# Optimization experiments

Hardware: AMD Instinct MI355X
Metric: run time of the kernel (lower is better)

## Reference

```python
import jax, jax.numpy as jnp
import numpy as np

B, T, C, H = 256, 256, 512, 64  # batch, seq, n_embd, head_size


def setup_inputs() -> dict:
    key = jax.random.key(0)
    kx, kk, kq, kv = jax.random.split(key, 4)
    x = jax.random.normal(kx, (B, T, C), dtype=jnp.float32)
    # nn.Linear(C, H, bias=False): store as [C, H] so y = x @ W
    Wk = jax.random.normal(kk, (C, H), dtype=jnp.float32) * (C ** -0.5)
    Wq = jax.random.normal(kq, (C, H), dtype=jnp.float32) * (C ** -0.5)
    Wv = jax.random.normal(kv, (C, H), dtype=jnp.float32) * (C ** -0.5)
    return {"x": x, "Wk": Wk, "Wq": Wq, "Wv": Wv}


def reference(x, Wk, Wq, Wv):
    Bx, Tx, Cx = x.shape
    k = jnp.einsum('btc,ch->bth', x, Wk)
    q = jnp.einsum('btc,ch->bth', x, Wq)
    v = jnp.einsum('btc,ch->bth', x, Wv)
    # NOTE: original scales by C**-0.5 (embed dim), not head_size**-0.5
    wei = jnp.einsum('bth,bsh->bts', q, k) * (Cx ** -0.5)  # [B,T,T]
    causal = jnp.tril(jnp.ones((Tx, Tx), dtype=bool))
    wei = jnp.where(causal, wei, -jnp.inf)
    wei = jax.nn.softmax(wei, axis=-1)
    # dropout is identity at inference (deterministic reference)
    out = jnp.einsum('bts,bsh->bth', wei, v)  # [B,T,H]
    return out
```

## Files before the change

kernel.cpp:

```cpp
#include <hip/hip_runtime.h>

#define BB 256
#define TT 256
#define CC 512
#define HH 64

typedef __bf16 bf16;
typedef __bf16 bf16x4 __attribute__((ext_vector_type(4)));
typedef __bf16 bf16x8 __attribute__((ext_vector_type(8)));
typedef float  f32x4  __attribute__((ext_vector_type(4)));

#define MFMA16(a, b, c) __builtin_amdgcn_mfma_f32_16x16x32_bf16((a), (b), (c), 0, 0, 0)

typedef __attribute__((address_space(1))) const void cas1_void;
typedef __attribute__((address_space(3))) void as3_void;
__device__ __forceinline__ void g2lds16(const void* g, void* l) {
    __builtin_amdgcn_global_load_lds((cas1_void*)g, (as3_void*)l, 16, 0, 0);
}

__global__ __launch_bounds__(256) void wtrans(const float* __restrict__ Wk,
                                              const float* __restrict__ Wq,
                                              const float* __restrict__ Wv,
                                              bf16* __restrict__ wt) {
    int which = blockIdx.y;
    const float* W = (which == 0) ? Wq : (which == 1) ? Wk : Wv;
    int idx = blockIdx.x * 256 + threadIdx.x;
    int n = idx & 63, k4 = idx >> 6;
    bf16x4 o;
    #pragma unroll
    for (int i = 0; i < 4; ++i) o[i] = (bf16)W[(k4 * 4 + i) * HH + n];
    *(bf16x4*)(&wt[which * (CC * HH) + n * CC + k4 * 4]) = o;
}

__global__ __launch_bounds__(1024) void fused(const float* __restrict__ x,
                                              const bf16* __restrict__ wt,
                                              float* __restrict__ out) {
    __shared__ __align__(16) char smem[135168];
    const int tid  = threadIdx.x;
    const int wv   = tid >> 6;
    const int lane = tid & 63;
    const int quad = lane >> 4;
    const int l15  = lane & 15;
    const int l7   = l15 & 7;
    const int l3   = l15 & 3;
    const int b    = blockIdx.x;
    const float* xg = x + (size_t)b * TT * CC;

    auto stage = [&](int p, int kc) {
        char* xbase = smem + p * 32768;
        #pragma unroll
        for (int j = 0; j < 2; ++j) {
            int s = j * 1024 + tid;
            int r = s >> 3, up = s & 7;
            int u = up ^ (r & 7);
            const float* gp = xg + (size_t)r * CC + kc * 32 + u * 4;
            g2lds16(gp, xbase + (j * 1024 + wv * 64) * 16);
        }
        if (wv < 12) {
            char* wbase = smem + 98304 + p * 12288;
            int n = wv * 16 + (lane >> 2);
            int u = (lane & 3) ^ (n & 3);
            const bf16* gp = wt + (size_t)n * CC + kc * 32 + u * 8;
            g2lds16(gp, wbase + wv * 1024);
        }
    };

    f32x4 acc[12];
    #pragma unroll
    for (int nt = 0; nt < 12; ++nt) acc[nt] = (f32x4){0.f, 0.f, 0.f, 0.f};

    stage(0, 0);
    int pc = 0;
    for (int kc = 0; kc < 16; ++kc) {
        int pn = (pc == 2) ? 0 : pc + 1;
        if (kc < 15) {
            stage(pn, kc + 1);
            if (wv < 12) asm volatile("s_waitcnt vmcnt(3)" ::: "memory");
            else         asm volatile("s_waitcnt vmcnt(2)" ::: "memory");
        } else {
            asm volatile("s_waitcnt vmcnt(0)" ::: "memory");
        }
        __builtin_amdgcn_s_barrier();

        const char* xbase = smem + pc * 32768;
        const char* wbase = smem + 98304 + pc * 12288;
        int row = wv * 16 + l15;
        const char* rp = xbase + row * 128;
        f32x4 x0 = *(const f32x4*)(rp + (((quad * 2)     ^ l7) * 16));
        f32x4 x1 = *(const f32x4*)(rp + (((quad * 2 + 1) ^ l7) * 16));
        bf16x8 a0;
        #pragma unroll
        for (int j = 0; j < 4; ++j) {
            a0[j] = (bf16)x0[j]; a0[j + 4] = (bf16)x1[j];
        }
        #pragma unroll
        for (int nt = 0; nt < 12; ++nt) {
            int n = (nt >> 2) * 64 + (nt & 3) * 16 + l15;
            const char* np = wbase + n * 64;
            bf16x8 b0 = *(const bf16x8*)(np + ((quad ^ l3) * 16));
            acc[nt] = MFMA16(a0, b0, acc[nt]);
        }
        pc = pn;
    }
    __syncthreads();

    bf16* qs = (bf16*)smem;
    bf16* ks = (bf16*)(smem + 32768);
    bf16* vs = (bf16*)(smem + 65536);
    const float scale = 0.044194173824159216f;
    {
        int gt = wv * 16 + quad * 4;
        #pragma unroll
        for (int nt = 0; nt < 12; ++nt) {
            int h = (nt & 3) * 16 + l15;
            int wch = nt >> 2;
            if (wch == 0) {
                #pragma unroll
                for (int r = 0; r < 4; ++r) {
                    int row = gt + r;
                    *(bf16*)((char*)qs + row * 128 + (((h >> 3) ^ (row & 7)) * 16)
                             + (h & 7) * 2) = (bf16)(acc[nt][r] * scale);
                }
            } else if (wch == 1) {
                #pragma unroll
                for (int r = 0; r < 4; ++r) {
                    int row = gt + r;
                    *(bf16*)((char*)ks + row * 128 + (((h >> 3) ^ (row & 7)) * 16)
                             + (h & 7) * 2) = (bf16)(acc[nt][r]);
                }
            } else {
                bf16x4 pv;
                #pragma unroll
                for (int r = 0; r < 4; ++r) pv[r] = (bf16)(acc[nt][r]);
                *(bf16x4*)((char*)vs + h * 512 + (((gt >> 3) ^ (h & 31)) * 16)
                           + ((gt >> 2) & 1) * 8) = pv;
            }
        }
    }
    __syncthreads();

    bf16* pb = (bf16*)(smem + 98304 + wv * 2048);
    const int w0 = wv & 1, w1 = (wv >> 1) & 1, w2 = (wv >> 2) & 1, w3 = wv >> 3;
    const int rt = (w3 << 3) | ((w1 ^ w3) << 2) | (w2 << 1) | (w0 ^ w2);
    const int rowbase = rt * 16;
    const int ctmax = rt;
    const int t = rowbase + l15;

    const char* qp = (const char*)qs + t * 128;
    bf16x8 bq0 = *(const bf16x8*)(qp + ((quad ^ l7) * 16));
    bf16x8 bq1 = *(const bf16x8*)(qp + (((4 + quad) ^ l7) * 16));

    float m_run = -3.0e38f, sm = 0.f;
    f32x4 o[4];
    #pragma unroll
    for (int ht = 0; ht < 4; ++ht) o[ht] = (f32x4){0.f, 0.f, 0.f, 0.f};

    #pragma unroll
    for (int qp4 = 0; qp4 < 4; ++qp4) {
        if (qp4 * 4 <= ctmax) {
            f32x4 sv[4];
            #pragma unroll
            for (int c2 = 0; c2 < 4; ++c2) {
                int ct = qp4 * 4 + c2;
                if (ct <= ctmax) {
                    const char* kp = (const char*)ks + (ct * 16 + l15) * 128;
                    bf16x8 k0 = *(const bf16x8*)(kp + ((quad ^ l7) * 16));
                    bf16x8 k1 = *(const bf16x8*)(kp + (((4 + quad) ^ l7) * 16));
                    f32x4 a = (f32x4){0.f, 0.f, 0.f, 0.f};
                    a = MFMA16(k0, bq0, a);
                    a = MFMA16(k1, bq1, a);
                    #pragma unroll
                    for (int r = 0; r < 4; ++r) {
                        int s = ct * 16 + quad * 4 + r;
                        sv[c2][r] = (s <= t) ? a[r] : -3.0e38f;
                    }
                }
            }
            float mq = -3.0e38f;
            #pragma unroll
            for (int c2 = 0; c2 < 4; ++c2)
                if (qp4 * 4 + c2 <= ctmax) {
                    #pragma unroll
                    for (int r = 0; r < 4; ++r) mq = fmaxf(mq, sv[c2][r]);
                }
            mq = fmaxf(mq, __shfl_xor(mq, 16));
            mq = fmaxf(mq, __shfl_xor(mq, 32));
            float mnew = fmaxf(m_run, mq);
            float alpha = __expf(m_run - mnew);
            sm *= alpha;
            #pragma unroll
            for (int ht = 0; ht < 4; ++ht)
                #pragma unroll
                for (int r = 0; r < 4; ++r) o[ht][r] *= alpha;
            m_run = mnew;

            #pragma unroll
            for (int c2 = 0; c2 < 4; ++c2) {
                int ct = qp4 * 4 + c2;
                if (ct <= ctmax) {
                    bf16x4 ev;
                    #pragma unroll
                    for (int r = 0; r < 4; ++r) {
                        float e = __expf(sv[c2][r] - m_run);
                        sm += e;
                        ev[r] = (bf16)e;
                    }
                    int u = 2 * c2 + (quad >> 1);
                    *(bf16x4*)((char*)pb + l15 * 128 + ((u ^ l7) * 16)
                               + (quad & 1) * 8) = ev;
                }
            }
            if (ctmax >= qp4 * 4 && ctmax < qp4 * 4 + 4 && !(ctmax & 1)) {
                int c2z = (ctmax & 3) + 1;
                int u = 2 * c2z + (quad >> 1);
                *(bf16x4*)((char*)pb + l15 * 128 + ((u ^ l7) * 16)
                           + (quad & 1) * 8) =
                    (bf16x4){(bf16)0.f, (bf16)0.f, (bf16)0.f, (bf16)0.f};
            }
            asm volatile("" ::: "memory");

            #pragma unroll
            for (int k2 = 0; k2 < 2; ++k2) {
                int ks2 = qp4 * 2 + k2;
                if (ks2 <= (ctmax >> 1)) {
                    int ur = 4 * k2 + quad;
                    bf16x8 pf = *(const bf16x8*)((char*)pb + l15 * 128
                                                 + ((ur ^ l7) * 16));
                    #pragma unroll
                    for (int ht = 0; ht < 4; ++ht) {
                        int vr = ht * 16 + l15;
                        bf16x8 vf = *(const bf16x8*)((const char*)vs + vr * 512
                                     + (((ks2 * 4 + quad) ^ (vr & 31)) * 16));
                        o[ht] = MFMA16(vf, pf, o[ht]);
                    }
                }
            }
            asm volatile("" ::: "memory");
        }
    }
    sm += __shfl_xor(sm, 16);
    sm += __shfl_xor(sm, 32);

    float rinv = 1.0f / sm;
    #pragma unroll
    for (int ht = 0; ht < 4; ++ht) {
        f32x4 ov;
        #pragma unroll
        for (int r = 0; r < 4; ++r) ov[r] = o[ht][r] * rinv;
        *(f32x4*)(&out[((size_t)b * TT + t) * HH + ht * 16 + quad * 4]) = ov;
    }
}

extern "C" void kernel_launch(void* const* d_in, const int* in_sizes, int n_in,
                              void* d_out, int out_size, void* d_ws, size_t ws_size,
                              hipStream_t stream) {
    const float* x  = (const float*)d_in[0];
    const float* Wk = (const float*)d_in[1];
    const float* Wq = (const float*)d_in[2];
    const float* Wv = (const float*)d_in[3];

    bf16* wt = (bf16*)d_ws;
    float* out = (float*)d_out;

    wtrans<<<dim3(32, 3), 256, 0, stream>>>(Wk, Wq, Wv, wt);
    fused<<<dim3(256), 1024, 0, stream>>>(x, wt, out);
}
```

Baseline: 209.6 us.

## Load x directly into registers instead of staging through LDS

Each wave now reads its x rows straight from global memory into registers, double-buffered with inline asm loads, instead of copying them into LDS with global_load_lds and reading them back. Only the bf16 weights still go through a triple-buffered LDS ring, which shrinks shared memory. The loop is fully unrolled with a sched_barrier so the hand-placed vmcnt waits still match. This removes the LDS write and read traffic for x, but the direct loads are less coalesced (each lane fetches 32 bytes from its own row) and the wait counts depend on exactly how many loads are issued.

```diff
diff --git a/kernel.cpp b/kernel.cpp
--- a/kernel.cpp
+++ b/kernel.cpp
@@ -16,6 +16,12 @@
 typedef __attribute__((address_space(3))) void as3_void;
 __device__ __forceinline__ void g2lds16(const void* g, void* l) {
     __builtin_amdgcn_global_load_lds((cas1_void*)g, (as3_void*)l, 16, 0, 0);
+}
+
+__device__ __forceinline__ f32x4 gload16(const float* p) {
+    f32x4 r;
+    asm volatile("global_load_dwordx4 %0, %1, off" : "=v"(r) : "v"(p) : "memory");
+    return r;
 }
 
 __global__ __launch_bounds__(256) void wtrans(const float* __restrict__ Wk,
@@ -35,7 +41,7 @@
 __global__ __launch_bounds__(1024) void fused(const float* __restrict__ x,
                                               const bf16* __restrict__ wt,
                                               float* __restrict__ out) {
-    __shared__ __align__(16) char smem[135168];
+    __shared__ __align__(16) char smem[131072];
     const int tid  = threadIdx.x;
     const int wv   = tid >> 6;
     const int lane = tid & 63;
@@ -46,18 +52,9 @@
     const int b    = blockIdx.x;
     const float* xg = x + (size_t)b * TT * CC;
 
-    auto stage = [&](int p, int kc) {
-        char* xbase = smem + p * 32768;
-        #pragma unroll
-        for (int j = 0; j < 2; ++j) {
-            int s = j * 1024 + tid;
-            int r = s >> 3, up = s & 7;
-            int u = up ^ (r & 7);
-            const float* gp = xg + (size_t)r * CC + kc * 32 + u * 4;
-            g2lds16(gp, xbase + (j * 1024 + wv * 64) * 16);
-        }
+    auto stage_wt = [&](int p, int kc) {
         if (wv < 12) {
-            char* wbase = smem + 98304 + p * 12288;
+            char* wbase = smem + p * 12288;
             int n = wv * 16 + (lane >> 2);
             int u = (lane & 3) ^ (n & 3);
             const bf16* gp = wt + (size_t)n * CC + kc * 32 + u * 8;
@@ -69,30 +66,42 @@
     #pragma unroll
     for (int nt = 0; nt < 12; ++nt) acc[nt] = (f32x4){0.f, 0.f, 0.f, 0.f};
 
-    stage(0, 0);
-    int pc = 0;
+    const float* xrow = xg + (size_t)(wv * 16 + l15) * CC + quad * 8;
+
+    f32x4 xA0, xA1, xB0, xB1;
+    xA0 = gload16(xrow);
+    xA1 = gload16(xrow + 4);
+    stage_wt(0, 0);
+
+    #pragma unroll
     for (int kc = 0; kc < 16; ++kc) {
-        int pn = (pc == 2) ? 0 : pc + 1;
+        const int pcl = kc % 3;
+        const bool even = ((kc & 1) == 0);
         if (kc < 15) {
-            stage(pn, kc + 1);
+            if (even) {
+                xB0 = gload16(xrow + (kc + 1) * 32);
+                xB1 = gload16(xrow + (kc + 1) * 32 + 4);
+            } else {
+                xA0 = gload16(xrow + (kc + 1) * 32);
+                xA1 = gload16(xrow + (kc + 1) * 32 + 4);
+            }
+            stage_wt((kc + 1) % 3, kc + 1);
             if (wv < 12) asm volatile("s_waitcnt vmcnt(3)" ::: "memory");
             else         asm volatile("s_waitcnt vmcnt(2)" ::: "memory");
         } else {
             asm volatile("s_waitcnt vmcnt(0)" ::: "memory");
         }
+        __builtin_amdgcn_sched_barrier(0);
         __builtin_amdgcn_s_barrier();
 
-        const char* xbase = smem + pc * 32768;
-        const char* wbase = smem + 98304 + pc * 12288;
-        int row = wv * 16 + l15;
-        const char* rp = xbase + row * 128;
-        f32x4 x0 = *(const f32x4*)(rp + (((quad * 2)     ^ l7) * 16));
-        f32x4 x1 = *(const f32x4*)(rp + (((quad * 2 + 1) ^ l7) * 16));
+        f32x4 c0 = even ? xA0 : xB0;
+        f32x4 c1 = even ? xA1 : xB1;
         bf16x8 a0;
         #pragma unroll
         for (int j = 0; j < 4; ++j) {
-            a0[j] = (bf16)x0[j]; a0[j + 4] = (bf16)x1[j];
-        }
+            a0[j] = (bf16)c0[j]; a0[j + 4] = (bf16)c1[j];
+        }
+        const char* wbase = smem + pcl * 12288;
         #pragma unroll
         for (int nt = 0; nt < 12; ++nt) {
             int n = (nt >> 2) * 64 + (nt & 3) * 16 + l15;
@@ -100,7 +109,6 @@
             bf16x8 b0 = *(const bf16x8*)(np + ((quad ^ l3) * 16));
             acc[nt] = MFMA16(a0, b0, acc[nt]);
         }
-        pc = pn;
     }
     __syncthreads();
 
```

New measurement: 212.2 us. About the same (+1.3%).
